# Kernel tuning notes

Hardware: AMD Instinct MI355X
Metric: run time of the kernel (lower is better)

## Reference

```python
import jax, jax.numpy as jnp
import numpy as np

B = 2
IMG = (128, 256, 256)
P = 16
E, NH, DH = 768, 12, 64
L, F = 12, 3072
WS = (512, 1024, 2048)   # LongNet segment lengths
RS = (1, 2, 4)           # matching dilation ratios
NEG = -1e9
NPATCH = (IMG[0] // P) * (IMG[1] // P) * (IMG[2] // P)
S = NPATCH + 1           # +1 CLS token


def setup_inputs() -> dict:
    key = jax.random.key(0)
    ks = jax.random.split(key, 16)
    def nrm(k, shape, std=0.02):
        return jax.random.normal(k, shape, jnp.float32) * std
    return {
        "x": jax.random.normal(ks[0], (B, 1) + IMG, jnp.float32),
        "conv_w": nrm(ks[1], (E, 1, P, P, P)),
        "conv_b": jnp.zeros((E,), jnp.float32),
        "cls_token": nrm(ks[2], (1, 1, E)),
        "pos_embed": nrm(ks[3], (1, S, E)),
        "ln1_g": jnp.ones((L, E)), "ln1_b": jnp.zeros((L, E)),
        "wq": nrm(ks[4], (L, E, E)), "bq": jnp.zeros((L, E)),
        "wk": nrm(ks[5], (L, E, E)), "bk": jnp.zeros((L, E)),
        "wv": nrm(ks[6], (L, E, E)), "bv": jnp.zeros((L, E)),
        "wo": nrm(ks[7], (L, E, E)), "bo": jnp.zeros((L, E)),
        "ln2_g": jnp.ones((L, E)), "ln2_b": jnp.zeros((L, E)),
        "w1": nrm(ks[8], (L, E, F)), "b1": jnp.zeros((L, F)),
        "w2": nrm(ks[9], (L, F, E)), "b2": jnp.zeros((L, E)),
        "normf_g": jnp.ones((E,)), "normf_b": jnp.zeros((E,)),
    }


def _ln(x, g, b, eps=1e-5):
    m = x.mean(-1, keepdims=True)
    v = ((x - m) ** 2).mean(-1, keepdims=True)
    return (x - m) * jax.lax.rsqrt(v + eps) * g + b


def _dilated_branch(q, k, v, w, r):
    # LongNet dilated attention for one (segment_length w, dilation r) config.
    # q,k,v: [B,S,H,d]. Head h uses offset h % r inside each segment of length w.
    b, s0, h, d = q.shape
    sp = -(-s0 // w) * w
    pad = sp - s0
    qp, kp, vp = (jnp.pad(t, ((0, 0), (0, pad), (0, 0), (0, 0))) for t in (q, k, v))
    n, m = sp // w, w // r
    idx = (jnp.arange(h)[:, None] % r) + jnp.arange(m)[None, :] * r      # [h,m]
    seg = lambda t: t.reshape(b, n, w, h, d).transpose(0, 1, 3, 2, 4)    # [b,n,h,w,d]
    gidx = idx[None, None, :, :, None]
    qs = jnp.take_along_axis(seg(qp), gidx, axis=3)                      # [b,n,h,m,d]
    ks = jnp.take_along_axis(seg(kp), gidx, axis=3)
    vs = jnp.take_along_axis(seg(vp), gidx, axis=3)
    kvalid = (jnp.arange(sp) < s0).reshape(n, w)[:, idx]                 # [n,h,m]
    scores = jnp.einsum('bnhqd,bnhkd->bnhqk', qs, ks) * (d ** -0.5)
    scores = jnp.where(kvalid[None, :, :, None, :], scores, NEG)
    lse = jax.nn.logsumexp(scores, axis=-1)                              # [b,n,h,m]
    out = jnp.einsum('bnhqk,bnhkd->bnhqd', jax.nn.softmax(scores, -1), vs)
    hh = jnp.arange(h)[:, None]
    out_f = jnp.zeros((b, n, h, w, d), q.dtype).at[:, :, hh, idx, :].set(out)
    lse_f = jnp.full((b, n, h, w), NEG, q.dtype).at[:, :, hh, idx].set(lse)
    return (out_f.transpose(0, 1, 3, 2, 4).reshape(b, sp, h, d),
            lse_f.transpose(0, 1, 3, 2).reshape(b, sp, h))


def _dilated_attention(q, k, v):
    # Combine branches weighted by softmax normalizers (exp lse), per LongNet.
    b, s0, h, d = q.shape
    smax = max(-(-s0 // w) * w for w in WS)
    outs, lses = [], []
    for w, r in zip(WS, RS):
        o, l = _dilated_branch(q, k, v, w, r)
        outs.append(jnp.pad(o, ((0, 0), (0, smax - o.shape[1]), (0, 0), (0, 0))))
        lses.append(jnp.pad(l, ((0, 0), (0, smax - l.shape[1]), (0, 0)),
                            constant_values=NEG))
    wgt = jax.nn.softmax(jnp.stack(lses), axis=0)[..., None]             # [nb,b,smax,h,1]
    out = (wgt * jnp.stack(outs)).sum(0)                                 # [b,smax,h,d]
    return out[:, :s0]


def reference(x, conv_w, conv_b, cls_token, pos_embed, ln1_g, ln1_b, wq, bq,
              wk, bk, wv, bv, wo, bo, ln2_g, ln2_b, w1, b1, w2, b2,
              normf_g, normf_b):
    b = x.shape[0]
    dp, hp, wp = IMG[0] // P, IMG[1] // P, IMG[2] // P
    # Conv3d patch embed with stride == kernel -> block reshape + matmul
    xp = x.reshape(b, 1, dp, P, hp, P, wp, P).transpose(0, 2, 4, 6, 1, 3, 5, 7)
    xp = xp.reshape(b, dp * hp * wp, -1) @ conv_w.reshape(E, -1).T + conv_b
    h = jnp.concatenate([jnp.broadcast_to(cls_token, (b, 1, E)), xp], axis=1)
    h = h + pos_embed  # seq length matches pos_embed, no interpolation needed

    def layer(hst, p):
        g1, lb1, Wq, Bq, Wk, Bk, Wv, Bv, Wo, Bo, g2, lb2, W1, B1, W2, B2 = p
        y = _ln(hst, g1, lb1)
        q = (y @ Wq + Bq).reshape(b, S, NH, DH)
        k = (y @ Wk + Bk).reshape(b, S, NH, DH)
        v = (y @ Wv + Bv).reshape(b, S, NH, DH)
        a = _dilated_attention(q, k, v).reshape(b, S, E) @ Wo + Bo
        hst = hst + a
        y = _ln(hst, g2, lb2)
        hst = hst + jax.nn.gelu(y @ W1 + B1, approximate=False) @ W2 + B2
        return hst, None

    params = (ln1_g, ln1_b, wq, bq, wk, bk, wv, bv, wo, bo,
              ln2_g, ln2_b, w1, b1, w2, b2)
    h, _ = jax.lax.scan(layer, h, params)
    h = _ln(h, normf_g, normf_b)
    return h[:, 0]
```

## Files before the change

kernel.cpp:

```cpp
#include <hip/hip_runtime.h>
#include <math.h>

#define SEQ 2049
#define EMB 768
#define NHEADS 12
#define QKVW 2304
#define MROWS 4098
#define MPAD 4224
#define NEGV -1000000000.0f

typedef short bs8 __attribute__((ext_vector_type(8)));
typedef float f4 __attribute__((ext_vector_type(4)));

__device__ __forceinline__ unsigned short f2bf(float f){
  union { float f; unsigned u; } x; x.f = f;
  unsigned r = x.u + 0x7fffu + ((x.u >> 16) & 1u);
  return (unsigned short)(r >> 16);
}
__device__ __forceinline__ unsigned short f2bf_fast(float f){
  union { float f; unsigned u; } x; x.f = f;
  return (unsigned short)((x.u + 0x8000u) >> 16);
}
__device__ __forceinline__ float bf2f(unsigned short u){
  union { unsigned u; float f; } x; x.u = ((unsigned)u) << 16; return x.f;
}

__device__ __forceinline__ float gelu_f(float x){
  float ax = fabsf(x)*0.70710678f;
  float t = 1.f/(1.f + 0.3275911f*ax);
  float p = t*(0.254829592f + t*(-0.284496736f + t*(1.421413741f
            + t*(-1.453152027f + t*1.061405429f))));
  float erfv = 1.f - p*__expf(-ax*ax);
  float s = (x >= 0.f) ? erfv : -erfv;
  return 0.5f*x*(1.f + s);
}

__device__ __forceinline__ void gl_lds16(const void* g, void* l){
  __builtin_amdgcn_global_load_lds((const __attribute__((address_space(1))) void*)g,
                                   (__attribute__((address_space(3))) void*)l, 16, 0, 0);
}

__global__ void wtr_k(const float* __restrict__ src, unsigned short* __restrict__ dst,
                      int K, int N, int LD, int NOFF)
{
  __shared__ float tile[32][33];
  int k0 = blockIdx.x*32, n0 = blockIdx.y*32, z = blockIdx.z;
  int tx = threadIdx.x, ty = threadIdx.y;
  const float* s = src + (size_t)z*K*N;
#pragma unroll
  for (int i=0;i<4;++i)
    tile[ty*4+i][tx] = s[(size_t)(k0+ty*4+i)*N + n0+tx];
  __syncthreads();
  unsigned short* dz = dst + ((size_t)z*LD + NOFF)*K;
#pragma unroll
  for (int i=0;i<4;++i)
    dz[(size_t)(n0+ty*4+i)*K + k0+tx] = f2bf(tile[tx][ty*4+i]);
}

__global__ void castconv_k(const float* __restrict__ src, unsigned short* __restrict__ dst){
  size_t i = ((size_t)blockIdx.x*256 + threadIdx.x)*4;
  float4 f = *(const float4*)(src+i);
  dst[i+0]=f2bf(f.x); dst[i+1]=f2bf(f.y); dst[i+2]=f2bf(f.z); dst[i+3]=f2bf(f.w);
}

__global__ void biascat_k(const float* __restrict__ bq, const float* __restrict__ bk,
                          const float* __restrict__ bv, float* __restrict__ dst){
  int i = blockIdx.x*256+threadIdx.x;
  int l = i/QKVW, c = i%QKVW;
  float v = (c<768) ? bq[l*768+c] : (c<1536 ? bk[l*768+c-768] : bv[l*768+c-1536]);
  dst[i] = v;
}

__global__ void patchify_k(const float* __restrict__ x, unsigned short* __restrict__ Xp)
{
  size_t gid = (size_t)blockIdx.x*256 + threadIdx.x;
  size_t oi = gid*4;
  int row = (int)(oi >> 12);
  int c = (int)(oi & 4095);
  int b = row >> 11; int p = row & 2047;
  int pd = p >> 8, ph = (p>>4)&15, pw = p&15;
  int pz = c >> 8, py = (c>>4)&15, px = c&15;
  size_t src = (((size_t)(b*128 + pd*16+pz)*256) + (size_t)(ph*16+py))*256 + (size_t)(pw*16+px);
  float4 f = *(const float4*)(x+src);
  Xp[oi+0]=f2bf(f.x); Xp[oi+1]=f2bf(f.y); Xp[oi+2]=f2bf(f.z); Xp[oi+3]=f2bf(f.w);
}

__global__ void assemble_k(const float* __restrict__ P, size_t pstride,
                           const float* __restrict__ cls,
                           const float* __restrict__ pos_e, float* __restrict__ H)
{
  int row = blockIdx.x; int t = threadIdx.x;
  float* hr = H + (size_t)row*EMB;
  if (row >= MROWS) { hr[t]=0.f; hr[t+256]=0.f; hr[t+512]=0.f; return; }
  int b = row / SEQ; int pos = row - b*SEQ;
#pragma unroll
  for (int c0=0;c0<3;++c0) {
    int c = t + c0*256;
    float v;
    if (pos==0) v = cls[c];
    else {
      size_t idx = ((size_t)(b*2048 + pos-1))*EMB + c;
      v = P[idx] + P[pstride+idx] + P[2*pstride+idx] + P[3*pstride+idx];
    }
    hr[c] = v + pos_e[(size_t)pos*EMB + c];
  }
}

__global__ __launch_bounds__(256) void ln_k(const float* __restrict__ H,
    const float* __restrict__ gam, const float* __restrict__ bet,
    unsigned short* __restrict__ Y)
{
  int row = blockIdx.x, t = threadIdx.x;
  const float* hr = H + (size_t)row*EMB;
  float v0 = hr[t], v1 = hr[t+256], v2 = hr[t+512];
  float s = v0+v1+v2;
#pragma unroll
  for (int off=32; off>=1; off>>=1) s += __shfl_down(s, off);
  __shared__ float r1[4], r2[4];
  if ((t&63)==0) r1[t>>6] = s;
  __syncthreads();
  float mean = (r1[0]+r1[1]+r1[2]+r1[3]) * (1.f/768.f);
  float d0=v0-mean, d1=v1-mean, d2=v2-mean;
  float q = d0*d0+d1*d1+d2*d2;
#pragma unroll
  for (int off=32; off>=1; off>>=1) q += __shfl_down(q, off);
  if ((t&63)==0) r2[t>>6] = q;
  __syncthreads();
  float rstd = rsqrtf((r2[0]+r2[1]+r2[2]+r2[3])*(1.f/768.f) + 1e-5f);
  unsigned short* yr = Y + (size_t)row*EMB;
  yr[t]     = f2bf(d0*rstd*gam[t]     + bet[t]);
  yr[t+256] = f2bf(d1*rstd*gam[t+256] + bet[t+256]);
  yr[t+512] = f2bf(d2*rstd*gam[t+512] + bet[t+512]);
}

template<int S>
__global__ __launch_bounds__(256) void ln_red_k(float* __restrict__ H,
    const float* __restrict__ P, size_t pstride,
    const float* __restrict__ gam, const float* __restrict__ bet,
    unsigned short* __restrict__ Y)
{
  int row = blockIdx.x, t = threadIdx.x;
  size_t base = (size_t)row*EMB;
  float v[3];
#pragma unroll
  for (int c0=0;c0<3;++c0) {
    size_t idx = base + t + c0*256;
    float h = H[idx];
#pragma unroll
    for (int s=0;s<S;++s) h += P[(size_t)s*pstride + idx];
    H[idx] = h; v[c0] = h;
  }
  float s = v[0]+v[1]+v[2];
#pragma unroll
  for (int off=32; off>=1; off>>=1) s += __shfl_down(s, off);
  __shared__ float r1[4], r2[4];
  if ((t&63)==0) r1[t>>6] = s;
  __syncthreads();
  float mean = (r1[0]+r1[1]+r1[2]+r1[3]) * (1.f/768.f);
  float d0=v[0]-mean, d1=v[1]-mean, d2=v[2]-mean;
  float q = d0*d0+d1*d1+d2*d2;
#pragma unroll
  for (int off=32; off>=1; off>>=1) q += __shfl_down(q, off);
  if ((t&63)==0) r2[t>>6] = q;
  __syncthreads();
  float rstd = rsqrtf((r2[0]+r2[1]+r2[2]+r2[3])*(1.f/768.f) + 1e-5f);
  unsigned short* yr = Y + base;
  yr[t]     = f2bf(d0*rstd*gam[t]     + bet[t]);
  yr[t+256] = f2bf(d1*rstd*gam[t+256] + bet[t+256]);
  yr[t+512] = f2bf(d2*rstd*gam[t+512] + bet[t+512]);
}

template<int S>
__global__ __launch_bounds__(256) void final_ln_red_k(const float* __restrict__ H,
   const float* __restrict__ P, size_t pstride,
   const float* __restrict__ gam, const float* __restrict__ bet, float* __restrict__ out)
{
  int b = blockIdx.x, t = threadIdx.x;
  size_t base = (size_t)(b*SEQ)*EMB;
  float v[3];
#pragma unroll
  for (int c0=0;c0<3;++c0) {
    size_t idx = base + t + c0*256;
    float h = H[idx];
#pragma unroll
    for (int s=0;s<S;++s) h += P[(size_t)s*pstride + idx];
    v[c0] = h;
  }
  float s = v[0]+v[1]+v[2];
#pragma unroll
  for (int off=32; off>=1; off>>=1) s += __shfl_down(s, off);
  __shared__ float r1[4], r2[4];
  if ((t&63)==0) r1[t>>6] = s;
  __syncthreads();
  float mean = (r1[0]+r1[1]+r1[2]+r1[3]) * (1.f/768.f);
  float d0=v[0]-mean, d1=v[1]-mean, d2=v[2]-mean;
  float q = d0*d0+d1*d1+d2*d2;
#pragma unroll
  for (int off=32; off>=1; off>>=1) q += __shfl_down(q, off);
  if ((t&63)==0) r2[t>>6] = q;
  __syncthreads();
  float rstd = rsqrtf((r2[0]+r2[1]+r2[2]+r2[3])*(1.f/768.f) + 1e-5f);
  out[b*EMB + t]     = d0*rstd*gam[t]     + bet[t];
  out[b*EMB + t+256] = d1*rstd*gam[t+256] + bet[t+256];
  out[b*EMB + t+512] = d2*rstd*gam[t+512] + bet[t+512];
}

template<int MODE, int NSPLIT>
__global__ __launch_bounds__(256) void gemm_k(
    const unsigned short* __restrict__ A,
    const unsigned short* __restrict__ Bt,
    const float* __restrict__ bias,
    unsigned short* __restrict__ Cb,
    float* __restrict__ Cf,
    int K, int ldc, size_t splitStride)
{
  __shared__ __attribute__((aligned(16))) unsigned short lA[3][128*32];
  __shared__ __attribute__((aligned(16))) unsigned short lB[3][128*32];
  const int tid = threadIdx.x;
  const int w = tid>>6, lane = tid&63, g = lane>>4, l16 = lane&15;
  const int lr = lane>>2;
  const int lcs = (((lane&3) ^ ((lane>>3)&3)))*8;
  const int swz = ((g ^ ((l16>>1)&3)))*8;
  const int nwg = gridDim.x*gridDim.y;
  const int id = blockIdx.y*gridDim.x + blockIdx.x;
  const int q = nwg>>3, r = nwg&7, xc = id&7, si = id>>3;
  const int nid = (xc<r ? xc*(q+1) : r*(q+1)+(xc-r)*q) + si;
  const int tm = nid / gridDim.x;
  const int tn = nid - tm*gridDim.x;
  const int kchunk = K / NSPLIT;
  const int kofs = (NSPLIT>1) ? blockIdx.z * kchunk : 0;
  const unsigned short* Ab = A + (size_t)tm*128*K + kofs;
  const unsigned short* Bb = Bt + (size_t)tn*128*K + kofs;
  const int wm = (w>>1)*64, wn = (w&1)*64;
  f4 acc[4][4] = {};
  const int nkt = kchunk>>5;

  auto STAGE = [&](int buf, int kt){
    const size_t ko = (size_t)(kt*32 + lcs);
    gl_lds16(Ab + (size_t)(w*16 + lr)*K + ko,     ((char*)lA[buf]) + w*1024);
    gl_lds16(Ab + (size_t)((w+4)*16 + lr)*K + ko, ((char*)lA[buf]) + (w+4)*1024);
    gl_lds16(Bb + (size_t)(w*16 + lr)*K + ko,     ((char*)lB[buf]) + w*1024);
    gl_lds16(Bb + (size_t)((w+4)*16 + lr)*K + ko, ((char*)lB[buf]) + (w+4)*1024);
  };

  STAGE(0, 0);
  STAGE(1, 1);
  for (int kt=0; kt<nkt; ++kt) {
    const int cur = kt % 3;
    if (kt+2 < nkt) {
      STAGE((kt+2)%3, kt+2);
      asm volatile("s_waitcnt vmcnt(8)" ::: "memory");
    } else if (kt+1 < nkt) {
      asm volatile("s_waitcnt vmcnt(4)" ::: "memory");
    } else {
      asm volatile("s_waitcnt vmcnt(0)" ::: "memory");
    }
    __builtin_amdgcn_sched_barrier(0);
    __builtin_amdgcn_s_barrier();
    bs8 af[4], bf[4];
#pragma unroll
    for (int mi=0;mi<4;++mi) af[mi] = *(const bs8*)(lA[cur] + (wm+mi*16+l16)*32 + swz);
#pragma unroll
    for (int ni=0;ni<4;++ni) bf[ni] = *(const bs8*)(lB[cur] + (wn+ni*16+l16)*32 + swz);
    asm volatile("s_waitcnt lgkmcnt(0)" ::: "memory");
    __builtin_amdgcn_sched_barrier(0);
    __builtin_amdgcn_s_barrier();
#pragma unroll
    for (int mi=0;mi<4;++mi)
#pragma unroll
      for (int ni=0;ni<4;++ni)
        acc[mi][ni] = __builtin_amdgcn_mfma_f32_16x16x32_bf16(af[mi], bf[ni], acc[mi][ni], 0,0,0);
  }
  const float bscale = (NSPLIT==1 || blockIdx.z==0) ? 1.f : 0.f;
#pragma unroll
  for (int mi=0;mi<4;++mi)
#pragma unroll
    for (int ni=0;ni<4;++ni) {
      int col = tn*128 + wn + ni*16 + l16;
      float bv = bias[col]*bscale;
#pragma unroll
      for (int r0=0;r0<4;++r0) {
        int row = tm*128 + wm + mi*16 + g*4 + r0;
        float val = acc[mi][ni][r0] + bv;
        if (MODE==1) val = gelu_f(val);
        if (MODE<=1) Cb[(size_t)row*ldc + col] = f2bf(val);
        else Cf[(size_t)blockIdx.z*splitStride + (size_t)row*ldc + col] = val;
      }
    }
}

__global__ __launch_bounds__(256) void attn_all_k(
    const unsigned short* __restrict__ qkv,
    unsigned short* __restrict__ O1, float* __restrict__ L1,
    unsigned short* __restrict__ O2, float* __restrict__ L2,
    unsigned short* __restrict__ O3, float* __restrict__ L3)
{
  __shared__ __attribute__((aligned(16))) unsigned short lK[128*72];
  __shared__ __attribute__((aligned(16))) unsigned short lVt[64*136];
  __shared__ __attribute__((aligned(16))) unsigned short Pl[4][16][136];
  const int tid = threadIdx.x;
  const int w = tid>>6, lane = tid&63, g = lane>>4, l16 = lane&15;

  int id = (blockIdx.x & 7)*240 + (blockIdx.x >> 3);
  int R, WSZ, NSEG; unsigned short* OB; float* LB;
  if (id < 960)       { R=1; WSZ=512;  NSEG=5; OB=O1; LB=L1; }
  else if (id < 1536) { id -= 960;  R=2; WSZ=1024; NSEG=3; OB=O2; LB=L2; }
  else                { id -= 1536; R=4; WSZ=2048; NSEG=2; OB=O3; LB=L3; }
  const int qt = id & 7; int rest = id >> 3;
  const int seg = rest % NSEG; const int bh = rest / NSEG;
  const int b = bh / NHEADS, hd = bh % NHEADS;
  const int hr = hd % R;
  const int j0 = qt*64 + w*16;
  const int kbase = seg*WSZ + hr;
  const unsigned short* qkvb = qkv + (size_t)b*SEQ*QKVW;

  bs8 z = {0,0,0,0,0,0,0,0};
  bs8 qf0 = z, qf1 = z;
  {
    int qpos = kbase + (j0 + l16)*R;
    if (qpos < SEQ) {
      const unsigned short* qrow = qkvb + (size_t)qpos*QKVW + hd*64 + g*8;
      qf0 = *(const bs8*)(qrow);
      qf1 = *(const bs8*)(qrow + 32);
    }
  }

  bs8 kreg[4], vreg[4];
  auto ISSUE = [&](int c){
#pragma unroll
    for (int it=0; it<4; ++it) {
      int idx = tid + it*256;
      int kkK = idx >> 3, dbK = idx & 7;
      int kposK = kbase + (c*128 + kkK)*R;
      bs8 kv = z;
      if (kposK < SEQ) kv = *(const bs8*)(qkvb + (size_t)kposK*QKVW + EMB + hd*64 + dbK*8);
      kreg[it] = kv;
      int kkV = idx & 127, dbV = idx >> 7;
      int kposV = kbase + (c*128 + kkV)*R;
      bs8 vv = z;
      if (kposV < SEQ) vv = *(const bs8*)(qkvb + (size_t)kposV*QKVW + 1536 + hd*64 + dbV*8);
      vreg[it] = vv;
    }
  };

  float rm[4], rs[4];
  f4 oacc[4] = {};
#pragma unroll
  for (int r=0;r<4;++r) { rm[r] = NEGV; rs[r] = 0.f; }

  ISSUE(0);
  for (int c=0; c<4; ++c) {
    __builtin_amdgcn_s_barrier();
#pragma unroll
    for (int it=0; it<4; ++it) {
      int idx = tid + it*256;
      int kkK = idx >> 3, dbK = idx & 7;
      *(bs8*)(lK + kkK*72 + dbK*8) = kreg[it];
      int kkV = idx & 127, dbV = idx >> 7;
#pragma unroll
      for (int ii=0; ii<8; ++ii) lVt[(dbV*8+ii)*136 + kkV] = (unsigned short)vreg[it][ii];
    }
    asm volatile("s_waitcnt lgkmcnt(0)" ::: "memory");
    __builtin_amdgcn_sched_barrier(0);
    __builtin_amdgcn_s_barrier();
    if (c+1 < 4) ISSUE(c+1);

    f4 sc[8];
#pragma unroll
    for (int kt=0; kt<8; ++kt) {
      int key = kt*16 + l16;
      bs8 kf0 = *(const bs8*)(lK + key*72 + g*8);
      bs8 kf1 = *(const bs8*)(lK + key*72 + 32 + g*8);
      f4 acc = {0.f,0.f,0.f,0.f};
      acc = __builtin_amdgcn_mfma_f32_16x16x32_bf16(qf0, kf0, acc, 0,0,0);
      acc = __builtin_amdgcn_mfma_f32_16x16x32_bf16(qf1, kf1, acc, 0,0,0);
      int kpos = kbase + (c*128 + key)*R;
      bool kvld = (kpos < SEQ);
#pragma unroll
      for (int r=0;r<4;++r) sc[kt][r] = kvld ? acc[r]*0.125f : NEGV;
    }
    float scl[4];
#pragma unroll
    for (int r=0;r<4;++r) {
      float mx = sc[0][r];
#pragma unroll
      for (int kt=1;kt<8;++kt) mx = fmaxf(mx, sc[kt][r]);
      mx = fmaxf(mx, __shfl_xor(mx, 1));
      mx = fmaxf(mx, __shfl_xor(mx, 2));
      mx = fmaxf(mx, __shfl_xor(mx, 4));
      mx = fmaxf(mx, __shfl_xor(mx, 8));
      float mn = fmaxf(rm[r], mx);
      scl[r] = __expf(rm[r] - mn);
      rm[r] = mn;
    }
#pragma unroll
    for (int r=0;r<4;++r) {
      float sm = 0.f;
#pragma unroll
      for (int kt=0;kt<8;++kt) { float p = __expf(sc[kt][r] - rm[r]); sc[kt][r] = p; sm += p; }
      sm += __shfl_xor(sm, 1); sm += __shfl_xor(sm, 2);
      sm += __shfl_xor(sm, 4); sm += __shfl_xor(sm, 8);
      rs[r] = rs[r]*scl[r] + sm;
    }
#pragma unroll
    for (int dt=0; dt<4; ++dt)
#pragma unroll
      for (int r=0;r<4;++r) oacc[dt][r] *= scl[r];
#pragma unroll
    for (int kt=0;kt<8;++kt)
#pragma unroll
      for (int r=0;r<4;++r)
        Pl[w][g*4+r][kt*16+l16] = f2bf_fast(sc[kt][r]);
#pragma unroll
    for (int ks=0; ks<4; ++ks) {
      bs8 pa = *(const bs8*)(&Pl[w][l16][ks*32 + g*8]);
#pragma unroll
      for (int dt=0; dt<4; ++dt) {
        bs8 vb = *(const bs8*)(lVt + (dt*16+l16)*136 + ks*32 + g*8);
        oacc[dt] = __builtin_amdgcn_mfma_f32_16x16x32_bf16(pa, vb, oacc[dt], 0,0,0);
      }
    }
  }

  size_t obase = ((size_t)(b*NSEG + seg)*NHEADS + hd)*512;
#pragma unroll
  for (int dt=0; dt<4; ++dt)
#pragma unroll
    for (int r=0;r<4;++r) {
      int j = j0 + g*4 + r;
      OB[(obase + j)*64 + dt*16 + l16] = f2bf(oacc[dt][r] / rs[r]);
    }
  if (l16 == 0) {
#pragma unroll
    for (int r=0;r<4;++r) LB[obase + j0 + g*4 + r] = rm[r] + __logf(rs[r]);
  }
}

__global__ __launch_bounds__(256) void attn_combine_k(
   const unsigned short* __restrict__ o1, const float* __restrict__ l1,
   const unsigned short* __restrict__ o2, const float* __restrict__ l2,
   const unsigned short* __restrict__ o3, const float* __restrict__ l3,
   unsigned short* __restrict__ attn)
{
  int row = blockIdx.x; int t = threadIdx.x;
  unsigned short* arow = attn + (size_t)row*EMB;
  if (row >= MROWS) { arow[t]=0; arow[t+256]=0; arow[t+512]=0; return; }
  int b = row / SEQ, pos = row - (row/SEQ)*SEQ;
#pragma unroll
  for (int c0=0; c0<3; ++c0) {
    int cc = t + c0*256;
    int hd = cc >> 6, d = cc & 63;
    float L0,L1v,L2v,O0,O1v,O2v;
    {
      int seg = pos >> 9; int j = pos & 511;
      size_t base = ((size_t)(b*5 + seg)*NHEADS + hd)*512 + j;
      L0 = l1[base]; O0 = bf2f(o1[base*64 + d]);
    }
    if ((pos & 1) == (hd & 1)) {
      int seg = pos >> 10; int j = ((pos & 1023) - (hd&1)) >> 1;
      size_t base = ((size_t)(b*3 + seg)*NHEADS + hd)*512 + j;
      L1v = l2[base]; O1v = bf2f(o2[base*64 + d]);
    } else { L1v = NEGV; O1v = 0.f; }
    if ((pos & 3) == (hd & 3)) {
      int seg = pos >> 11; int j = ((pos & 2047) - (hd&3)) >> 2;
      size_t base = ((size_t)(b*2 + seg)*NHEADS + hd)*512 + j;
      L2v = l3[base]; O2v = bf2f(o3[base*64 + d]);
    } else { L2v = NEGV; O2v = 0.f; }
    float m = fmaxf(L0, fmaxf(L1v, L2v));
    float e0 = __expf(L0-m), e1 = __expf(L1v-m), e2 = __expf(L2v-m);
    float inv = 1.f/(e0+e1+e2);
    arow[cc] = f2bf((e0*O0+e1*O1v+e2*O2v)*inv);
  }
}

extern "C" void kernel_launch(void* const* d_in, const int* in_sizes, int n_in,
                              void* d_out, int out_size, void* d_ws, size_t ws_size,
                              hipStream_t stream) {
  const float* x       = (const float*)d_in[0];
  const float* conv_w  = (const float*)d_in[1];
  const float* conv_b  = (const float*)d_in[2];
  const float* cls     = (const float*)d_in[3];
  const float* pos_e   = (const float*)d_in[4];
  const float* ln1_g   = (const float*)d_in[5];
  const float* ln1_b   = (const float*)d_in[6];
  const float* wq      = (const float*)d_in[7];
  const float* bq      = (const float*)d_in[8];
  const float* wk      = (const float*)d_in[9];
  const float* bk      = (const float*)d_in[10];
  const float* wv      = (const float*)d_in[11];
  const float* bv      = (const float*)d_in[12];
  const float* wo      = (const float*)d_in[13];
  const float* bo      = (const float*)d_in[14];
  const float* ln2_g   = (const float*)d_in[15];
  const float* ln2_b   = (const float*)d_in[16];
  const float* w1      = (const float*)d_in[17];
  const float* b1      = (const float*)d_in[18];
  const float* w2      = (const float*)d_in[19];
  const float* b2      = (const float*)d_in[20];
  const float* nf_g    = (const float*)d_in[21];
  const float* nf_b    = (const float*)d_in[22];

  char* ws = (char*)d_ws;
  size_t off = 0;
  auto alloc = [&](size_t bytes)->char* {
    char* p = ws + off; off += (bytes + 255) & ~(size_t)255; return p;
  };
  unsigned short* wqkv_t = (unsigned short*)alloc((size_t)12*2304*768*2);
  unsigned short* wo_t   = (unsigned short*)alloc((size_t)12*768*768*2);
  unsigned short* w1_t   = (unsigned short*)alloc((size_t)12*3072*768*2);
  unsigned short* w2_t   = (unsigned short*)alloc((size_t)12*768*3072*2);
  unsigned short* cw_b   = (unsigned short*)alloc((size_t)768*4096*2);
  float* bqkv            = (float*)alloc((size_t)12*2304*4);
  unsigned short* Xp     = (unsigned short*)alloc((size_t)4096*4096*2);
  float* H               = (float*)alloc((size_t)MPAD*768*4);
  float* P               = (float*)alloc((size_t)4*MPAD*768*4);
  unsigned short* Y      = (unsigned short*)alloc((size_t)MPAD*768*2);
  unsigned short* QKV    = (unsigned short*)alloc((size_t)MPAD*2304*2);
  unsigned short* ATT    = (unsigned short*)alloc((size_t)MPAD*768*2);
  unsigned short* Y2     = (unsigned short*)alloc((size_t)MPAD*3072*2);
  unsigned short* O1 = (unsigned short*)alloc((size_t)2*5*12*512*64*2);
  unsigned short* O2 = (unsigned short*)alloc((size_t)2*3*12*512*64*2);
  unsigned short* O3 = (unsigned short*)alloc((size_t)2*2*12*512*64*2);
  float* L1 = (float*)alloc((size_t)2*5*12*512*4);
  float* L2 = (float*)alloc((size_t)2*3*12*512*4);
  float* L3 = (float*)alloc((size_t)2*2*12*512*4);
  const size_t PSTR = (size_t)MPAD*768;

  dim3 tb(32,8);
  wtr_k<<<dim3(24,24,12), tb, 0, stream>>>(wq, wqkv_t, 768, 768, 2304, 0);
  wtr_k<<<dim3(24,24,12), tb, 0, stream>>>(wk, wqkv_t, 768, 768, 2304, 768);
  wtr_k<<<dim3(24,24,12), tb, 0, stream>>>(wv, wqkv_t, 768, 768, 2304, 1536);
  wtr_k<<<dim3(24,24,12), tb, 0, stream>>>(wo, wo_t, 768, 768, 768, 0);
  wtr_k<<<dim3(24,96,12), tb, 0, stream>>>(w1, w1_t, 768, 3072, 3072, 0);
  wtr_k<<<dim3(96,24,12), tb, 0, stream>>>(w2, w2_t, 3072, 768, 768, 0);
  castconv_k<<<3072,256,0,stream>>>(conv_w, cw_b);
  biascat_k<<<108,256,0,stream>>>(bq,bk,bv,bqkv);
  patchify_k<<<16384,256,0,stream>>>(x, Xp);
  gemm_k<3,4><<<dim3(6,32,4),256,0,stream>>>(Xp, cw_b, conv_b, nullptr, P, 4096, 768, PSTR);
  assemble_k<<<MPAD,256,0,stream>>>(P, PSTR, cls, pos_e, H);

  for (int l=0;l<12;++l) {
    if (l==0) ln_k<<<MPAD,256,0,stream>>>(H, ln1_g, ln1_b, Y);
    else ln_red_k<2><<<MPAD,256,0,stream>>>(H, P, PSTR, ln1_g + l*768, ln1_b + l*768, Y);
    gemm_k<0,1><<<dim3(18,33),256,0,stream>>>(Y, wqkv_t + (size_t)l*2304*768, bqkv + l*2304, QKV, nullptr, 768, 2304, 0);
    attn_all_k<<<1920,256,0,stream>>>(QKV, O1,L1,O2,L2,O3,L3);
    attn_combine_k<<<MPAD,256,0,stream>>>(O1,L1,O2,L2,O3,L3, ATT);
    gemm_k<3,2><<<dim3(6,33,2),256,0,stream>>>(ATT, wo_t + (size_t)l*768*768, bo + l*768, nullptr, P, 768, 768, PSTR);
    ln_red_k<2><<<MPAD,256,0,stream>>>(H, P, PSTR, ln2_g + l*768, ln2_b + l*768, Y);
    gemm_k<1,1><<<dim3(24,33),256,0,stream>>>(Y, w1_t + (size_t)l*3072*768, b1 + l*3072, Y2, nullptr, 768, 3072, 0);
    gemm_k<3,2><<<dim3(6,33,2),256,0,stream>>>(Y2, w2_t + (size_t)l*768*3072, b2 + l*768, nullptr, P, 3072, 768, PSTR);
  }
  final_ln_red_k<2><<<2,256,0,stream>>>(H, P, PSTR, nf_g, nf_b, (float*)d_out);
}
```

Baseline: 2.856 ms.

## Skip fully-padded attention tiles and trim key chunks in dilated attention

```diff
diff --git a/kernel.cpp b/kernel.cpp
--- a/kernel.cpp
+++ b/kernel.cpp
@@ -310,11 +310,23 @@
   const int seg = rest % NSEG; const int bh = rest / NSEG;
   const int b = bh / NHEADS, hd = bh % NHEADS;
   const int hr = hd % R;
+  const int kbase = seg*WSZ + hr;
+  bs8 z = {0,0,0,0,0,0,0,0};
+
+  if (kbase + qt*64*R >= SEQ) {
+    size_t ob2 = ((size_t)(b*NSEG + seg)*NHEADS + hd)*512 + qt*64;
+    int row = tid>>2, cb = (tid&3)*16;
+    *(bs8*)(&OB[(ob2 + row)*64 + cb])     = z;
+    *(bs8*)(&OB[(ob2 + row)*64 + cb + 8]) = z;
+    if (tid < 64) LB[ob2 + tid] = NEGV;
+    return;
+  }
+  int nvk = (SEQ - 1 - kbase)/R + 1; if (nvk > 512) nvk = 512;
+  const int nck = (nvk + 127) >> 7;
+
   const int j0 = qt*64 + w*16;
-  const int kbase = seg*WSZ + hr;
   const unsigned short* qkvb = qkv + (size_t)b*SEQ*QKVW;
 
-  bs8 z = {0,0,0,0,0,0,0,0};
   bs8 qf0 = z, qf1 = z;
   {
     int qpos = kbase + (j0 + l16)*R;
@@ -325,22 +337,32 @@
     }
   }
 
+  const int dbK = tid&7, kkKb = tid>>3;
+  const int kkV = tid&127, dbV0 = tid>>7;
+  const unsigned short* pK = qkvb + (size_t)(kbase + kkKb*R)*QKVW + EMB + hd*64 + dbK*8;
+  const unsigned short* pV = qkvb + (size_t)(kbase + kkV*R)*QKVW + 1536 + hd*64 + dbV0*8;
+  const size_t stepIt = (size_t)32*R*QKVW;
+  const size_t stepC  = (size_t)128*R*QKVW;
+  int ci = 0;
   bs8 kreg[4], vreg[4];
-  auto ISSUE = [&](int c){
-#pragma unroll
-    for (int it=0; it<4; ++it) {
-      int idx = tid + it*256;
-      int kkK = idx >> 3, dbK = idx & 7;
-      int kposK = kbase + (c*128 + kkK)*R;
-      bs8 kv = z;
-      if (kposK < SEQ) kv = *(const bs8*)(qkvb + (size_t)kposK*QKVW + EMB + hd*64 + dbK*8);
-      kreg[it] = kv;
-      int kkV = idx & 127, dbV = idx >> 7;
-      int kposV = kbase + (c*128 + kkV)*R;
-      bs8 vv = z;
-      if (kposV < SEQ) vv = *(const bs8*)(qkvb + (size_t)kposV*QKVW + 1536 + hd*64 + dbV*8);
-      vreg[it] = vv;
-    }
+  auto ISSUE = [&](){
+    const bool full = (kbase + (ci*128 + 127)*R) < SEQ;
+    if (full) {
+#pragma unroll
+      for (int it=0; it<4; ++it) kreg[it] = *(const bs8*)(pK + (size_t)it*stepIt);
+#pragma unroll
+      for (int it=0; it<4; ++it) vreg[it] = *(const bs8*)(pV + it*16);
+    } else {
+      const int cofs = ci*128*R;
+#pragma unroll
+      for (int it=0; it<4; ++it)
+        kreg[it] = (kbase + (kkKb + it*32)*R + cofs < SEQ)
+                   ? *(const bs8*)(pK + (size_t)it*stepIt) : z;
+      const bool vv = (kbase + kkV*R + cofs) < SEQ;
+#pragma unroll
+      for (int it=0; it<4; ++it) vreg[it] = vv ? *(const bs8*)(pV + it*16) : z;
+    }
+    pK += stepC; pV += stepC; ++ci;
   };
 
   float rm[4], rs[4];
@@ -348,24 +370,21 @@
 #pragma unroll
   for (int r=0;r<4;++r) { rm[r] = NEGV; rs[r] = 0.f; }
 
-  ISSUE(0);
-  for (int c=0; c<4; ++c) {
-    __builtin_amdgcn_s_barrier();
+  ISSUE();
+  for (int c=0; c<nck; ++c) {
+    __syncthreads();
 #pragma unroll
     for (int it=0; it<4; ++it) {
-      int idx = tid + it*256;
-      int kkK = idx >> 3, dbK = idx & 7;
-      *(bs8*)(lK + kkK*72 + dbK*8) = kreg[it];
-      int kkV = idx & 127, dbV = idx >> 7;
-#pragma unroll
-      for (int ii=0; ii<8; ++ii) lVt[(dbV*8+ii)*136 + kkV] = (unsigned short)vreg[it][ii];
-    }
-    asm volatile("s_waitcnt lgkmcnt(0)" ::: "memory");
-    __builtin_amdgcn_sched_barrier(0);
-    __builtin_amdgcn_s_barrier();
-    if (c+1 < 4) ISSUE(c+1);
-
+      *(bs8*)(lK + (kkKb + it*32)*72 + dbK*8) = kreg[it];
+#pragma unroll
+      for (int ii=0; ii<8; ++ii) lVt[((dbV0+it*2)*8+ii)*136 + kkV] = (unsigned short)vreg[it][ii];
+    }
+    __syncthreads();
+    if (c+1 < nck) ISSUE();
+
+    const bool fullc = (kbase + (c*128 + 127)*R) < SEQ;
     f4 sc[8];
+    __builtin_amdgcn_s_setprio(1);
 #pragma unroll
     for (int kt=0; kt<8; ++kt) {
       int key = kt*16 + l16;
@@ -374,10 +393,21 @@
       f4 acc = {0.f,0.f,0.f,0.f};
       acc = __builtin_amdgcn_mfma_f32_16x16x32_bf16(qf0, kf0, acc, 0,0,0);
       acc = __builtin_amdgcn_mfma_f32_16x16x32_bf16(qf1, kf1, acc, 0,0,0);
-      int kpos = kbase + (c*128 + key)*R;
-      bool kvld = (kpos < SEQ);
-#pragma unroll
-      for (int r=0;r<4;++r) sc[kt][r] = kvld ? acc[r]*0.125f : NEGV;
+      sc[kt] = acc;
+    }
+    __builtin_amdgcn_s_setprio(0);
+    if (fullc) {
+#pragma unroll
+      for (int kt=0; kt<8; ++kt)
+#pragma unroll
+        for (int r=0;r<4;++r) sc[kt][r] *= 0.125f;
+    } else {
+#pragma unroll
+      for (int kt=0; kt<8; ++kt) {
+        bool kvld = (kbase + (c*128 + kt*16 + l16)*R) < SEQ;
+#pragma unroll
+        for (int r=0;r<4;++r) sc[kt][r] = kvld ? sc[kt][r]*0.125f : NEGV;
+      }
     }
     float scl[4];
 #pragma unroll
@@ -398,19 +428,20 @@
       float sm = 0.f;
 #pragma unroll
       for (int kt=0;kt<8;++kt) { float p = __expf(sc[kt][r] - rm[r]); sc[kt][r] = p; sm += p; }
-      sm += __shfl_xor(sm, 1); sm += __shfl_xor(sm, 2);
-      sm += __shfl_xor(sm, 4); sm += __shfl_xor(sm, 8);
       rs[r] = rs[r]*scl[r] + sm;
     }
-#pragma unroll
-    for (int dt=0; dt<4; ++dt)
-#pragma unroll
-      for (int r=0;r<4;++r) oacc[dt][r] *= scl[r];
+    if (scl[0]<1.f || scl[1]<1.f || scl[2]<1.f || scl[3]<1.f) {
+#pragma unroll
+      for (int dt=0; dt<4; ++dt)
+#pragma unroll
+        for (int r=0;r<4;++r) oacc[dt][r] *= scl[r];
+    }
 #pragma unroll
     for (int kt=0;kt<8;++kt)
 #pragma unroll
       for (int r=0;r<4;++r)
         Pl[w][g*4+r][kt*16+l16] = f2bf_fast(sc[kt][r]);
+    __builtin_amdgcn_s_setprio(1);
 #pragma unroll
     for (int ks=0; ks<4; ++ks) {
       bs8 pa = *(const bs8*)(&Pl[w][l16][ks*32 + g*8]);
@@ -420,6 +451,15 @@
         oacc[dt] = __builtin_amdgcn_mfma_f32_16x16x32_bf16(pa, vb, oacc[dt], 0,0,0);
       }
     }
+    __builtin_amdgcn_s_setprio(0);
+  }
+
+#pragma unroll
+  for (int r=0;r<4;++r) {
+    float s = rs[r];
+    s += __shfl_xor(s, 1); s += __shfl_xor(s, 2);
+    s += __shfl_xor(s, 4); s += __shfl_xor(s, 8);
+    rs[r] = s;
   }
 
   size_t obase = ((size_t)(b*NSEG + seg)*NHEADS + hd)*512;
```

Result: faster. 2.738 ms (-4.1%).
